# Kernel optimization log

Measured on AMD Instinct MI355X. Metric: run time of the kernel, lower is better.

## Reference

```python
import jax, jax.numpy as jnp
import numpy as np

EPSILON = 0.1  # adversarial perturbation magnitude (q = 1 norm)
N_HIDDEN1 = 4096


def setup_inputs() -> dict:
    key = jax.random.key(0)
    ks = jax.random.split(key, 6)
    batch, n_in, n_hid, n_out = 4096, 2048, N_HIDDEN1, 1024
    x = jax.random.normal(ks[0], (batch, n_in), dtype=jnp.float32)
    y = jax.random.normal(ks[1], (batch, n_out), dtype=jnp.float32)
    # AdvLinearNet params: beta ~ U[0,1)/sqrt(n_out), bias = 0
    beta = jax.random.uniform(ks[2], (n_in, n_out), dtype=jnp.float32) / np.sqrt(n_out)
    bias_lin = jnp.zeros((n_out,), dtype=jnp.float32)
    # AdvOneLayer params (gamma = 1.0): W1 = -U/ (gamma*n_hid), W2 = U/(gamma*n_out)
    W1 = -jax.random.uniform(ks[3], (n_hid, n_in), dtype=jnp.float32) / n_hid
    W2 = jax.random.uniform(ks[4], (n_out, n_hid), dtype=jnp.float32) / n_out
    bias1 = jnp.zeros((n_hid,), dtype=jnp.float32)
    bias2 = jnp.zeros((n_out,), dtype=jnp.float32)
    return {"x": x, "y": y, "beta": beta, "bias_lin": bias_lin,
            "W1": W1, "W2": W2, "bias1": bias1, "bias2": bias2, "adv": 1}


def reference(x, y, beta, bias_lin, W1, W2, bias1, bias2, adv):
    # ---- AdvLinearNet ----
    lin = jnp.matmul(x, beta) + bias_lin            # [B, n_out]
    if adv:
        # torch.norm(beta, dim=0, p=1) -> per-output-column L1 norm
        beta_norm = jnp.sum(jnp.abs(beta), axis=0)  # [n_out]
        lin = lin - EPSILON * y * beta_norm
    # ---- AdvOneLayer ----
    if adv:
        # Faithful to source: summand = W2[i, j] * n_hidden1 (the relu hidden
        # computation inside the double loop is dead code), so the adv output
        # is constant across the batch.
        one = N_HIDDEN1 * jnp.sum(W2, axis=1) + bias2      # [n_out]
        one = jnp.broadcast_to(one, lin.shape)             # [B, n_out]
    else:
        h = jax.nn.relu(jnp.matmul(x, W1.T) + bias1)       # [B, n_hid]
        one = jnp.matmul(h, W2.T) + bias2                  # [B, n_out]
    return lin + one
```

## Files before the change

kernel.cpp:

```cpp
#include <hip/hip_runtime.h>
#include <hip/hip_bf16.h>


typedef float    f32x4  __attribute__((ext_vector_type(4)));
typedef unsigned u32x4  __attribute__((ext_vector_type(4)));
typedef long     lx2    __attribute__((ext_vector_type(2)));

constexpr int M = 4096;
constexpr int N = 1024;
constexpr int K = 2048;
constexpr int NHID = 4096;

__device__ __forceinline__ unsigned pk4f8(float a, float b, float c, float d) {
    unsigned v = __builtin_amdgcn_cvt_pk_fp8_f32(a, b, 0, false);
    v = __builtin_amdgcn_cvt_pk_fp8_f32(c, d, v, true);
    return v;
}

__device__ __forceinline__ void gll16(const void* g, void* l) {
    __builtin_amdgcn_global_load_lds(
        (const __attribute__((address_space(1))) void*)g,
        (__attribute__((address_space(3))) void*)l, 16, 0, 0);
}

__global__ void __launch_bounds__(256) pre_kernel(
    const float* __restrict__ x, const float* __restrict__ beta,
    const float* __restrict__ W2,
    char* __restrict__ xb, char* __restrict__ bt,
    float* __restrict__ partials,
    float* __restrict__ wsum) {
    __shared__ float tls[64 * 132];
    const int bx = blockIdx.x, tid = threadIdx.x;
    if (bx < 1024) {
        const int rt = bx >> 4, kt = bx & 15;
        {
            const int r = tid >> 2, c0 = (tid & 3) * 32;
            const float* src = x + (size_t)(rt * 64 + r) * K + kt * 128 + c0;
            #pragma unroll
            for (int i = 0; i < 8; ++i)
                *(f32x4*)&tls[r * 132 + c0 + i * 4] = *(const f32x4*)(src + i * 4);
        }
        __syncthreads();
        {
            const int r = tid >> 2;
            const float* row = &tls[r * 132];
            char* orow = xb + (size_t)(rt * 64 + r) * K + kt * 128;
            #pragma unroll
            for (int uu = 0; uu < 2; ++uu) {
                const int u = (tid & 3) + uu * 4;
                const int p = u >> 2, q = u & 3;
                const float* h0 = row + p * 64 + q * 8;
                const float* h1 = h0 + 32;
                u32x4 o = { pk4f8(h0[0], h0[1], h0[2], h0[3]),
                            pk4f8(h0[4], h0[5], h0[6], h0[7]),
                            pk4f8(h1[0], h1[1], h1[2], h1[3]),
                            pk4f8(h1[4], h1[5], h1[6], h1[7]) };
                *(u32x4*)(orow + u * 16) = o;
            }
        }
    } else if (bx < 1536) {
        const int tile = bx - 1024, tk = tile & 31, tn = tile >> 5;
        {
            const int r = tid >> 2, c0 = (tid & 3) * 16;
            const float* src = beta + (size_t)(tk * 64 + r) * N + tn * 64 + c0;
            #pragma unroll
            for (int j = 0; j < 4; ++j)
                *(f32x4*)&tls[r * 68 + c0 + j * 4] = *(const f32x4*)(src + j * 4);
        }
        __syncthreads();
        {
            const int n = tid >> 2, q = tid & 3;
            float s = 0.f;
            float v0[8], v1[8];
            #pragma unroll
            for (int j = 0; j < 8; ++j) {
                v0[j] = tls[(q * 8 + j) * 68 + n];
                v1[j] = tls[(32 + q * 8 + j) * 68 + n];
                s += fabsf(v0[j]) + fabsf(v1[j]);
            }
            s += __shfl_xor(s, 1);
            s += __shfl_xor(s, 2);
            if (q == 0) partials[tk * 1024 + tn * 64 + n] = s;
            u32x4 o = { pk4f8(v0[0], v0[1], v0[2], v0[3]),
                        pk4f8(v0[4], v0[5], v0[6], v0[7]),
                        pk4f8(v1[0], v1[1], v1[2], v1[3]),
                        pk4f8(v1[4], v1[5], v1[6], v1[7]) };
            *(u32x4*)(bt + (size_t)(tn * 64 + n) * K + tk * 64 + q * 16) = o;
        }
    } else {
        const int b = bx - 1536;
        const int wv = tid >> 6, lane = tid & 63;
        const int row = b * 4 + wv;
        const f32x4* w4 = (const f32x4*)(W2 + (size_t)row * NHID);
        float acc = 0.f;
        #pragma unroll
        for (int i = 0; i < 16; ++i) {
            f32x4 v = w4[i * 64 + lane];
            acc += v[0] + v[1] + v[2] + v[3];
        }
        #pragma unroll
        for (int off = 32; off; off >>= 1) acc += __shfl_down(acc, off);
        if (lane == 0) wsum[row] = acc;
    }
}

constexpr int BKu = 128;
constexpr int NT  = K / BKu;
constexpr int ASZ = 128 * BKu;
constexpr int BSZ = 64 * BKu;

__global__ void __launch_bounds__(512, 4) gemm_kernel(
    const char* __restrict__ xb, const char* __restrict__ bt,
    const float* __restrict__ y,
    const float* __restrict__ partials, const float* __restrict__ wsum,
    const float* __restrict__ bias_lin, const float* __restrict__ bias2,
    float* __restrict__ out) {
    __shared__ __align__(16) char Al[3 * ASZ];
    __shared__ __align__(16) char Bl[3 * BSZ];

    const int tid = threadIdx.x, lane = tid & 63, w = tid >> 6;
    const int wm = w >> 1, wn = w & 1;
    const int c = blockIdx.x & 7, local = blockIdx.x >> 3;
    const int mb = ((c & 1) << 4) + (local >> 2);
    const int nb = ((c >> 1) << 2) + (local & 3);
    const int brow = mb * 128, bcol = nb * 64;

    const int srow = lane >> 3;
    const int sulog = (lane & 7) ^ srow;
    const char* asrc0 = xb + (size_t)(brow + w * 16 + srow) * K + sulog * 16;
    const char* asrc1 = asrc0 + (size_t)8 * K;
    const char* bsrc  = bt + (size_t)(bcol + w * 8 + srow) * K + sulog * 16;

    auto STAGE = [&](int buf, int t) {
        gll16(asrc0 + t * BKu, &Al[buf * ASZ + w * 2048]);
        gll16(asrc1 + t * BKu, &Al[buf * ASZ + w * 2048 + 1024]);
        gll16(bsrc  + t * BKu, &Bl[buf * BSZ + w * 1024]);
    };

    const int r = lane & 15, q = lane >> 4;
    int aoff[2][2], boff[2][2];
    #pragma unroll
    for (int m = 0; m < 2; ++m)
        #pragma unroll
        for (int p = 0; p < 2; ++p) {
            const int row = wm * 32 + m * 16 + r;
            aoff[m][p] = row * 128 + (((p * 4 + q) ^ (r & 7)) * 16);
        }
    #pragma unroll
    for (int n = 0; n < 2; ++n)
        #pragma unroll
        for (int p = 0; p < 2; ++p) {
            const int row = wn * 32 + n * 16 + r;
            boff[n][p] = row * 128 + (((p * 4 + q) ^ (r & 7)) * 16);
        }

    f32x4 acc[2][2];
    #pragma unroll
    for (int m = 0; m < 2; ++m)
        #pragma unroll
        for (int n = 0; n < 2; ++n) acc[m][n] = (f32x4)0.f;

    auto COMPUTE = [&](int buf) {
        const char* A = &Al[buf * ASZ];
        const char* B = &Bl[buf * BSZ];
        #pragma unroll
        for (int p = 0; p < 2; ++p) {
            lx2 a0 = *(const lx2*)&A[aoff[0][p]];
            lx2 a1 = *(const lx2*)&A[aoff[1][p]];
            lx2 b0 = *(const lx2*)&B[boff[0][p]];
            lx2 b1 = *(const lx2*)&B[boff[1][p]];
            acc[0][0] = __builtin_amdgcn_mfma_f32_16x16x32_fp8_fp8(a0.x, b0.x, acc[0][0], 0, 0, 0);
            acc[0][1] = __builtin_amdgcn_mfma_f32_16x16x32_fp8_fp8(a0.x, b1.x, acc[0][1], 0, 0, 0);
            acc[1][0] = __builtin_amdgcn_mfma_f32_16x16x32_fp8_fp8(a1.x, b0.x, acc[1][0], 0, 0, 0);
            acc[1][1] = __builtin_amdgcn_mfma_f32_16x16x32_fp8_fp8(a1.x, b1.x, acc[1][1], 0, 0, 0);
            acc[0][0] = __builtin_amdgcn_mfma_f32_16x16x32_fp8_fp8(a0.y, b0.y, acc[0][0], 0, 0, 0);
            acc[0][1] = __builtin_amdgcn_mfma_f32_16x16x32_fp8_fp8(a0.y, b1.y, acc[0][1], 0, 0, 0);
            acc[1][0] = __builtin_amdgcn_mfma_f32_16x16x32_fp8_fp8(a1.y, b0.y, acc[1][0], 0, 0, 0);
            acc[1][1] = __builtin_amdgcn_mfma_f32_16x16x32_fp8_fp8(a1.y, b1.y, acc[1][1], 0, 0, 0);
        }
    };

    STAGE(0, 0);
    STAGE(1, 1);
    for (int t = 0; t < NT; ++t) {
        if (t < NT - 1) { asm volatile("s_waitcnt vmcnt(3)" ::: "memory"); }
        else            { asm volatile("s_waitcnt vmcnt(0)" ::: "memory"); }
        __builtin_amdgcn_s_barrier();
        __builtin_amdgcn_sched_barrier(0);
        if (t + 2 < NT) STAGE((t + 2) % 3, t + 2);
        COMPUTE(t % 3);
    }

    #pragma unroll
    for (int n = 0; n < 2; ++n) {
        const int gc = bcol + wn * 32 + n * 16 + r;
        float bsum = 0.f;
        #pragma unroll 8
        for (int tk = 0; tk < 32; ++tk) bsum += partials[tk * 1024 + gc];
        const float be = 0.1f * bsum;
        const float ct = bias_lin[gc] + bias2[gc] + (float)NHID * wsum[gc];
        #pragma unroll
        for (int m = 0; m < 2; ++m) {
            const int gr0 = brow + wm * 32 + m * 16 + q * 4;
            f32x4 v = acc[m][n];
            #pragma unroll
            for (int rr = 0; rr < 4; ++rr) {
                size_t idx = (size_t)(gr0 + rr) * N + gc;
                out[idx] = v[rr] + ct - be * y[idx];
            }
        }
    }
}

extern "C" void kernel_launch(void* const* d_in, const int* in_sizes, int n_in,
                              void* d_out, int out_size, void* d_ws, size_t ws_size,
                              hipStream_t stream) {
    const float* x        = (const float*)d_in[0];
    const float* y        = (const float*)d_in[1];
    const float* beta     = (const float*)d_in[2];
    const float* bias_lin = (const float*)d_in[3];
    const float* W2       = (const float*)d_in[5];
    const float* bias2    = (const float*)d_in[7];
    float* out = (float*)d_out;

    float* partials = (float*)d_ws;
    float* wsum     = partials + 32 * 1024;
    char*  xb       = (char*)(wsum + 1024);
    char*  bts      = xb + (size_t)M * K;

    pre_kernel<<<1792, 256, 0, stream>>>(x, beta, W2, xb, bts, partials, wsum);
    gemm_kernel<<<512, 512, 0, stream>>>(xb, bts, y, partials, wsum,
                                         bias_lin, bias2, out);
}
```

Baseline: 36.08 us.

## Enlarge GEMM block tile to 128x128 with split A/B staging and priority scheduling

Each block now computes a 128x128 output tile with a 2x4 wave layout and 4x2 MFMA tiles per wave, halving the grid to 256 blocks and raising operand reuse per LDS load. The loop splits each K-step into two half-steps that interleave A and B global-to-LDS staging with register-prefetched LDS reads. It also wraps the MFMA bursts in s_setprio. The aim is less LDS and global traffic per FLOP and better overlap of memory with compute. In exchange the grid becomes 256 blocks, which may underfill the GPU's compute units, and there are more barriers per iteration.

```diff
diff --git a/kernel.cpp b/kernel.cpp
--- a/kernel.cpp
+++ b/kernel.cpp
@@ -106,44 +106,46 @@
 
 constexpr int BKu = 128;
 constexpr int NT  = K / BKu;
-constexpr int ASZ = 128 * BKu;
-constexpr int BSZ = 64 * BKu;
-
-__global__ void __launch_bounds__(512, 4) gemm_kernel(
+constexpr int TSZ = 128 * BKu;
+
+__global__ void __launch_bounds__(512, 2) gemm_kernel(
     const char* __restrict__ xb, const char* __restrict__ bt,
     const float* __restrict__ y,
     const float* __restrict__ partials, const float* __restrict__ wsum,
     const float* __restrict__ bias_lin, const float* __restrict__ bias2,
     float* __restrict__ out) {
-    __shared__ __align__(16) char Al[3 * ASZ];
-    __shared__ __align__(16) char Bl[3 * BSZ];
+    __shared__ __align__(16) char Al[3 * TSZ];
+    __shared__ __align__(16) char Bl[3 * TSZ];
 
     const int tid = threadIdx.x, lane = tid & 63, w = tid >> 6;
-    const int wm = w >> 1, wn = w & 1;
+    const int wm = w >> 2, wn = w & 3;
     const int c = blockIdx.x & 7, local = blockIdx.x >> 3;
-    const int mb = ((c & 1) << 4) + (local >> 2);
-    const int nb = ((c >> 1) << 2) + (local & 3);
-    const int brow = mb * 128, bcol = nb * 64;
-
-    const int srow = lane >> 3;
-    const int sulog = (lane & 7) ^ srow;
-    const char* asrc0 = xb + (size_t)(brow + w * 16 + srow) * K + sulog * 16;
-    const char* asrc1 = asrc0 + (size_t)8 * K;
-    const char* bsrc  = bt + (size_t)(bcol + w * 8 + srow) * K + sulog * 16;
-
-    auto STAGE = [&](int buf, int t) {
-        gll16(asrc0 + t * BKu, &Al[buf * ASZ + w * 2048]);
-        gll16(asrc1 + t * BKu, &Al[buf * ASZ + w * 2048 + 1024]);
-        gll16(bsrc  + t * BKu, &Bl[buf * BSZ + w * 1024]);
+    const int mb = (c << 2) + (local >> 3);
+    const int nb = local & 7;
+    const int brow = mb * 128, bcol = nb * 128;
+
+    const int schk = (tid & 7) ^ ((tid >> 3) & 7);
+    const char* asrc = xb + (size_t)(brow + (tid >> 3)) * K + schk * 16;
+    const char* bsrc = bt + (size_t)(bcol + (tid >> 3)) * K + schk * 16;
+
+    auto STAGE_A = [&](int buf, int t) {
+        gll16(asrc + (size_t)t * BKu, &Al[buf * TSZ + tid * 16]);
+        gll16(asrc + (size_t)64 * K + (size_t)t * BKu,
+              &Al[buf * TSZ + 8192 + tid * 16]);
     };
+    auto STAGE_B = [&](int buf, int t) {
+        gll16(bsrc + (size_t)t * BKu, &Bl[buf * TSZ + tid * 16]);
+        gll16(bsrc + (size_t)64 * K + (size_t)t * BKu,
+              &Bl[buf * TSZ + 8192 + tid * 16]);
+    };
 
     const int r = lane & 15, q = lane >> 4;
-    int aoff[2][2], boff[2][2];
-    #pragma unroll
-    for (int m = 0; m < 2; ++m)
+    int aoff[4][2], boff[2][2];
+    #pragma unroll
+    for (int m = 0; m < 4; ++m)
         #pragma unroll
         for (int p = 0; p < 2; ++p) {
-            const int row = wm * 32 + m * 16 + r;
+            const int row = wm * 64 + m * 16 + r;
             aoff[m][p] = row * 128 + (((p * 4 + q) ^ (r & 7)) * 16);
         }
     #pragma unroll
@@ -154,41 +156,76 @@
             boff[n][p] = row * 128 + (((p * 4 + q) ^ (r & 7)) * 16);
         }
 
-    f32x4 acc[2][2];
-    #pragma unroll
-    for (int m = 0; m < 2; ++m)
+    f32x4 acc[4][2];
+    #pragma unroll
+    for (int m = 0; m < 4; ++m)
         #pragma unroll
         for (int n = 0; n < 2; ++n) acc[m][n] = (f32x4)0.f;
 
-    auto COMPUTE = [&](int buf) {
-        const char* A = &Al[buf * ASZ];
-        const char* B = &Bl[buf * BSZ];
-        #pragma unroll
-        for (int p = 0; p < 2; ++p) {
-            lx2 a0 = *(const lx2*)&A[aoff[0][p]];
-            lx2 a1 = *(const lx2*)&A[aoff[1][p]];
-            lx2 b0 = *(const lx2*)&B[boff[0][p]];
-            lx2 b1 = *(const lx2*)&B[boff[1][p]];
-            acc[0][0] = __builtin_amdgcn_mfma_f32_16x16x32_fp8_fp8(a0.x, b0.x, acc[0][0], 0, 0, 0);
-            acc[0][1] = __builtin_amdgcn_mfma_f32_16x16x32_fp8_fp8(a0.x, b1.x, acc[0][1], 0, 0, 0);
-            acc[1][0] = __builtin_amdgcn_mfma_f32_16x16x32_fp8_fp8(a1.x, b0.x, acc[1][0], 0, 0, 0);
-            acc[1][1] = __builtin_amdgcn_mfma_f32_16x16x32_fp8_fp8(a1.x, b1.x, acc[1][1], 0, 0, 0);
-            acc[0][0] = __builtin_amdgcn_mfma_f32_16x16x32_fp8_fp8(a0.y, b0.y, acc[0][0], 0, 0, 0);
-            acc[0][1] = __builtin_amdgcn_mfma_f32_16x16x32_fp8_fp8(a0.y, b1.y, acc[0][1], 0, 0, 0);
-            acc[1][0] = __builtin_amdgcn_mfma_f32_16x16x32_fp8_fp8(a1.y, b0.y, acc[1][0], 0, 0, 0);
-            acc[1][1] = __builtin_amdgcn_mfma_f32_16x16x32_fp8_fp8(a1.y, b1.y, acc[1][1], 0, 0, 0);
-        }
-    };
-
-    STAGE(0, 0);
-    STAGE(1, 1);
+    STAGE_A(0, 0); STAGE_B(0, 0);
+    STAGE_A(1, 1); STAGE_B(1, 1);
+    asm volatile("s_waitcnt vmcnt(4)" ::: "memory");
+    __builtin_amdgcn_s_barrier();
+
+    int b0 = 0, b1 = 1, b2 = 2;
     for (int t = 0; t < NT; ++t) {
-        if (t < NT - 1) { asm volatile("s_waitcnt vmcnt(3)" ::: "memory"); }
-        else            { asm volatile("s_waitcnt vmcnt(0)" ::: "memory"); }
-        __builtin_amdgcn_s_barrier();
+        const char* A = &Al[b0 * TSZ];
+        const char* B = &Bl[b0 * TSZ];
+
+        lx2 pa[4], pb[2];
+        #pragma unroll
+        for (int m = 0; m < 4; ++m) pa[m] = *(const lx2*)&A[aoff[m][0]];
+        #pragma unroll
+        for (int n = 0; n < 2; ++n) pb[n] = *(const lx2*)&B[boff[n][0]];
+        if (t + 2 < NT) STAGE_A(b2, t + 2);
+        __builtin_amdgcn_s_barrier();
+        asm volatile("s_waitcnt lgkmcnt(0)" ::: "memory");
         __builtin_amdgcn_sched_barrier(0);
-        if (t + 2 < NT) STAGE((t + 2) % 3, t + 2);
-        COMPUTE(t % 3);
+        __builtin_amdgcn_s_setprio(1);
+        #pragma unroll
+        for (int m = 0; m < 4; ++m)
+            #pragma unroll
+            for (int n = 0; n < 2; ++n)
+                acc[m][n] = __builtin_amdgcn_mfma_f32_16x16x32_fp8_fp8(
+                    pa[m].x, pb[n].x, acc[m][n], 0, 0, 0);
+        #pragma unroll
+        for (int m = 0; m < 4; ++m)
+            #pragma unroll
+            for (int n = 0; n < 2; ++n)
+                acc[m][n] = __builtin_amdgcn_mfma_f32_16x16x32_fp8_fp8(
+                    pa[m].y, pb[n].y, acc[m][n], 0, 0, 0);
+        __builtin_amdgcn_s_setprio(0);
+        __builtin_amdgcn_s_barrier();
+
+        #pragma unroll
+        for (int m = 0; m < 4; ++m) pa[m] = *(const lx2*)&A[aoff[m][1]];
+        #pragma unroll
+        for (int n = 0; n < 2; ++n) pb[n] = *(const lx2*)&B[boff[n][1]];
+        if (t + 2 < NT) STAGE_B(b2, t + 2);
+        __builtin_amdgcn_s_barrier();
+        asm volatile("s_waitcnt lgkmcnt(0)" ::: "memory");
+        __builtin_amdgcn_sched_barrier(0);
+        __builtin_amdgcn_s_setprio(1);
+        #pragma unroll
+        for (int m = 0; m < 4; ++m)
+            #pragma unroll
+            for (int n = 0; n < 2; ++n)
+                acc[m][n] = __builtin_amdgcn_mfma_f32_16x16x32_fp8_fp8(
+                    pa[m].x, pb[n].x, acc[m][n], 0, 0, 0);
+        #pragma unroll
+        for (int m = 0; m < 4; ++m)
+            #pragma unroll
+            for (int n = 0; n < 2; ++n)
+                acc[m][n] = __builtin_amdgcn_mfma_f32_16x16x32_fp8_fp8(
+                    pa[m].y, pb[n].y, acc[m][n], 0, 0, 0);
+        __builtin_amdgcn_s_setprio(0);
+        if (t < NT - 1) {
+            if (t + 2 < NT) { asm volatile("s_waitcnt vmcnt(4)" ::: "memory"); }
+            else            { asm volatile("s_waitcnt vmcnt(0)" ::: "memory"); }
+        }
+        __builtin_amdgcn_s_barrier();
+
+        const int tmp = b0; b0 = b1; b1 = b2; b2 = tmp;
     }
 
     #pragma unroll
@@ -200,8 +237,8 @@
         const float be = 0.1f * bsum;
         const float ct = bias_lin[gc] + bias2[gc] + (float)NHID * wsum[gc];
         #pragma unroll
-        for (int m = 0; m < 2; ++m) {
-            const int gr0 = brow + wm * 32 + m * 16 + q * 4;
+        for (int m = 0; m < 4; ++m) {
+            const int gr0 = brow + wm * 64 + m * 16 + q * 4;
             f32x4 v = acc[m][n];
             #pragma unroll
             for (int rr = 0; rr < 4; ++rr) {
@@ -229,6 +266,6 @@
     char*  bts      = xb + (size_t)M * K;
 
     pre_kernel<<<1792, 256, 0, stream>>>(x, beta, W2, xb, bts, partials, wsum);
-    gemm_kernel<<<512, 512, 0, stream>>>(xb, bts, y, partials, wsum,
+    gemm_kernel<<<256, 512, 0, stream>>>(xb, bts, y, partials, wsum,
                                          bias_lin, bias2, out);
 }
```

Result: slower. 40.64 us (+12.7%).
